# Optimization experiments

Hardware: AMD Instinct MI355X
Metric: run time of the kernel (lower is better)

## Reference

```python
import jax, jax.numpy as jnp
import numpy as np

B = 65536
F = 300                      # length of each frequency response function
SIGMA = 2.0                  # gaussian blur stdev (init arg)
SCALE = 1.0                  # scale_factor
ALPHA = 1.0                  # softlocalmax sharpness (default)
I0, I1 = 100.0, 200.0        # interval passed to __init__
PMAX = F // 2 + 1            # max possible number of strict local maxima (incl. boundary peaks)


def _gauss_kernel(sigma):
    l = int(np.round(3.0 * sigma + 1.0))
    x = np.linspace(-(l - 1.0) / 2.0, (l - 1.0) / 2.0, l)
    k = np.exp(-0.5 * np.square(x) / np.square(sigma))
    return jnp.asarray(k / k.sum(), dtype=jnp.float32)


def _freqs_norm():
    # freqs = arange(1,301) normalized by interval to (-1,1)-centered coords
    f = np.arange(1, F + 1, dtype=np.float32)
    f = (f - I0) / (I1 - I0)
    return jnp.asarray(f * 2.0 - 1.0)


def setup_inputs() -> dict:
    key = jax.random.key(0)
    fr_funcs = jax.random.normal(key, (B, F), dtype=jnp.float32)
    return {"fr_funcs": fr_funcs}


def _forward(fr):
    kernel = _gauss_kernel(SIGMA)
    freqs = _freqs_norm()

    # Gaussian1DBlur: conv1d with symmetric kernel, zero 'same' padding
    f = jax.lax.conv_general_dilated(fr[:, None, :], kernel[None, None, :],
                                     (1,), "SAME")[:, 0, :]  # (B,F)

    # --- peak detection, equivalent to scipy.find_peaks on a width-2
    # symmetric-padded signal: strict interior maxima plus boundary peaks ---
    interior = (f[:, 1:-1] > f[:, :-2]) & (f[:, 1:-1] > f[:, 2:])   # (B,F-2)
    is_peak = jnp.concatenate([f[:, :1] > f[:, 1:2], interior,
                               f[:, -1:] > f[:, -2:-1]], axis=1)    # (B,F)
    P = is_peak.sum(axis=1)                 # number of peaks per row
    nseg = jnp.maximum(P, 1)                # P=0 still yields one segment [0,F-1)

    idx = jnp.arange(F)
    # sorted peak positions, padded with sentinel F
    pos = jnp.sort(jnp.where(is_peak, idx, F), axis=1)[:, :PMAX]    # (B,PMAX)
    # interval dividers = floor midpoints of consecutive peaks (int(start/end) truncation)
    mids = jnp.where(pos[:, 1:] < F, (pos[:, :-1] + pos[:, 1:]) // 2, F)  # (B,PMAX-1)

    # element i in [0,F-1) belongs to segment = #mids <= i  (last index F-1 excluded,
    # exactly as function[int(start):int(end)] with final divider F-1)
    elem_idx = jnp.arange(F - 1)
    seg_id = jax.vmap(lambda m: jnp.searchsorted(m, elem_idx, side="right"))(mids)  # (B,F-1)

    rows = jnp.arange(B)[:, None] * PMAX
    seg_flat = (seg_id + rows).reshape(-1)
    vals = f[:, : F - 1].reshape(-1)
    frq = jnp.broadcast_to(freqs[: F - 1], (B, F - 1)).reshape(-1)
    NS = B * PMAX

    # per-segment stable softmax-weighted frequency (softargmax)
    segmax = jax.ops.segment_max(vals, seg_flat, num_segments=NS)
    w = jnp.exp((vals - segmax[seg_flat]) * ALPHA)
    den = jax.ops.segment_sum(w, seg_flat, num_segments=NS)
    num = jax.ops.segment_sum(w * frq, seg_flat, num_segments=NS)
    sm = (num / jnp.where(den > 0, den, 1.0)).reshape(B, PMAX)      # (B,PMAX)

    valid = jnp.arange(PMAX)[None, :] < nseg[:, None]
    neg_sq = -(sm * sm)                     # midpoint of normalized interval (-1,1) is 0
    in_int = valid & (sm > -1.0) & (sm < 1.0)

    sum_in = jnp.sum(jnp.where(in_int, neg_sq, 0.0), axis=1)
    # no peak in interval: sum of the two largest -(peak-mid)^2 among valid peaks
    top2 = jax.lax.top_k(jnp.where(valid, neg_sq, -jnp.inf), 2)[0]
    top2sum = jnp.sum(jnp.where(jnp.isfinite(top2), top2, 0.0), axis=1)

    return jnp.where(in_int.any(axis=1), sum_in, top2sum) * SCALE   # (B,)


def reference(fr_funcs):
    return _forward(fr_funcs)
```

## Files before the change

### kernel.cpp

```cpp
#include <hip/hip_runtime.h>
#include <cmath>


constexpr int FLEN = 300;
constexpr int RPB  = 4;
constexpr int SMAX = 152;

__global__ __launch_bounds__(256, 8)
void pil_kernel(const float* __restrict__ in, float* __restrict__ out,
                double bk0, double bk1, double bk2, double bk3)
{
    const int w    = threadIdx.x >> 6;
    const int lane = threadIdx.x & 63;
    const int row  = blockIdx.x * RPB + w;

    __shared__ double2        eg_s[RPB][FLEN];
    __shared__ unsigned short ps_s[RPB][SMAX];

    double2*        eg = eg_s[w];
    unsigned short* ps = ps_s[w];

    const float* rin  = in + (size_t)row * FLEN;
    const int    base = lane * 5;
    const bool   act  = (lane < 60);
    const int    bC   = act ? base : 295;

    float r0 = rin[bC+0], r1 = rin[bC+1], r2 = rin[bC+2], r3 = rin[bC+3], r4 = rin[bC+4];
    float l2 = __shfl_up(r2, 1), l3 = __shfl_up(r3, 1), l4 = __shfl_up(r4, 1);
    float h0 = __shfl_down(r0, 1), h1 = __shfl_down(r1, 1), h2 = __shfl_down(r2, 1);
    if (lane == 0)  { l2 = 0.f; l3 = 0.f; l4 = 0.f; }
    if (lane >= 59) { h0 = 0.f; h1 = 0.f; h2 = 0.f; }

    const double d0=(double)l2, d1=(double)l3, d2=(double)l4, d3=(double)r0,
                 d4=(double)r1, d5=(double)r2, d6=(double)r3, d7=(double)r4,
                 d8=(double)h0, d9=(double)h1, d10=(double)h2;
    float f[5];
    f[0] = (float)fma(bk0, d0+d6,  fma(bk1, d1+d5, fma(bk2, d2+d4, bk3*d3)));
    f[1] = (float)fma(bk0, d1+d7,  fma(bk1, d2+d6, fma(bk2, d3+d5, bk3*d4)));
    f[2] = (float)fma(bk0, d2+d8,  fma(bk1, d3+d7, fma(bk2, d4+d6, bk3*d5)));
    f[3] = (float)fma(bk0, d3+d9,  fma(bk1, d4+d8, fma(bk2, d5+d7, bk3*d6)));
    f[4] = (float)fma(bk0, d4+d10, fma(bk1, d5+d9, fma(bk2, d6+d8, bk3*d7)));

    float fm1 = __shfl_up(f[4], 1);
    float fp1 = __shfl_down(f[0], 1);
    if (lane == 0)  fm1 = -__builtin_inff();
    if (lane >= 59) fp1 = -__builtin_inff();

    bool p[5];
    {
        float lft = fm1;
        #pragma unroll
        for (int j = 0; j < 5; ++j) {
            float rgt = (j < 4) ? f[j+1] : fp1;
            p[j] = act && (f[j] > lft) && (f[j] > rgt);
            lft = f[j];
        }
    }

    unsigned long long b0 = __ballot(p[0]), b1 = __ballot(p[1]), b2 = __ballot(p[2]),
                       b3 = __ballot(p[3]), b4 = __ballot(p[4]);
    const unsigned long long below = (1ull << lane) - 1ull;
    int off = __popcll(b0 & below) + __popcll(b1 & below) + __popcll(b2 & below)
            + __popcll(b3 & below) + __popcll(b4 & below);
    const int P = __popcll(b0) + __popcll(b1) + __popcll(b2) + __popcll(b3) + __popcll(b4);
    #pragma unroll
    for (int j = 0; j < 5; ++j)
        if (p[j]) ps[off++] = (unsigned short)(base + j);

    float e5[5], fr5[5];
    double tE = 0.0, tG = 0.0;
    #pragma unroll
    for (int j = 0; j < 5; ++j) {
        int  i = base + j;
        bool v = act && (i < FLEN - 1);
        e5[j]  = v ? __expf(f[j]) : 0.f;
        fr5[j] = fmaf((float)(i - 99), 0.02f, -1.0f);
        tE += (double)e5[j];
        tG  = fma((double)e5[j], (double)fr5[j], tG);
    }

    double sE = tE, sG = tG;
    #pragma unroll
    for (int d = 1; d < 64; d <<= 1) {
        double a = __shfl_up(sE, d), b = __shfl_up(sG, d);
        if (lane >= d) { sE += a; sG += b; }
    }

    double runE = sE - tE, runG = sG - tG;
    if (lane == 63) eg[0] = make_double2(0.0, 0.0);
    #pragma unroll
    for (int j = 0; j < 5; ++j) {
        int i = base + j;
        runE += (double)e5[j];
        runG  = fma((double)e5[j], (double)fr5[j], runG);
        if (act && i <= FLEN - 2)
            eg[i + 1] = make_double2(runE, runG);
    }
    __syncthreads();

    const int nseg = (P > 0) ? P : 1;
    float sum_in = 0.f; int any_in = 0;
    float nsq_l[3]; int nsq_n = 0;
    for (int s = lane; s < nseg; s += 64) {
        int im = (s > 0) ? s - 1 : 0;
        int ip = (s < P - 1) ? s + 1 : im;
        int pm = ps[im], pc = ps[(P > 0) ? s : 0], pn = ps[ip];
        int lo = (s == 0)        ? 0        : ((pm + pc) >> 1);
        int hi = (s == nseg - 1) ? FLEN - 1 : ((pc + pn) >> 1);
        double2 a = eg[lo], b = eg[hi];
        float den = (float)(b.x - a.x);
        float num = (float)(b.y - a.y);
        float sm  = num / den;
        float nsq = -(sm * sm);
        bool  ii  = (sm > -1.0f) && (sm < 1.0f);
        if (ii) { sum_in += nsq; any_in = 1; }
        if (nsq_n < 3) nsq_l[nsq_n] = nsq;
        nsq_n += 1;
    }

    if (__ballot(any_in) != 0ull) {
        #pragma unroll
        for (int d = 32; d >= 1; d >>= 1) sum_in += __shfl_xor(sum_in, d);
        if (lane == 0) out[row] = sum_in;
    } else {
        float m1 = -__builtin_inff(), m2 = -__builtin_inff();
        for (int q = 0; q < nsq_n; ++q) {
            float nsq = nsq_l[q];
            if (nsq > m1) { m2 = m1; m1 = nsq; } else { m2 = fmaxf(m2, nsq); }
        }
        #pragma unroll
        for (int d = 32; d >= 1; d >>= 1) {
            float o1 = __shfl_xor(m1, d);
            float o2 = __shfl_xor(m2, d);
            float n1 = fmaxf(m1, o1);
            float n2 = fmaxf(fminf(m1, o1), fmaxf(m2, o2));
            m1 = n1; m2 = n2;
        }
        if (lane == 0) {
            float t2 = m1 + ((m2 > -__builtin_inff()) ? m2 : 0.0f);
            out[row] = t2;
        }
    }
}

extern "C" void kernel_launch(void* const* d_in, const int* in_sizes, int n_in,
                              void* d_out, int out_size, void* d_ws, size_t ws_size,
                              hipStream_t stream) {
    const float* in  = (const float*)d_in[0];
    float*       out = (float*)d_out;
    const int B = in_sizes[0] / FLEN;

    double k[7], s = 0.0;
    for (int t = 0; t < 7; ++t) {
        double x = -3.0 + (double)t;
        k[t] = exp(-0.5 * x * x / 4.0);
        s += k[t];
    }
    double bk0 = (double)(float)(k[0] / s);
    double bk1 = (double)(float)(k[1] / s);
    double bk2 = (double)(float)(k[2] / s);
    double bk3 = (double)(float)(k[3] / s);

    pil_kernel<<<B / RPB, 256, 0, stream>>>(in, out, bk0, bk1, bk2, bk3);
}
```

Baseline: 126.8 us.

## Replace block barrier with wave-level sync, shrink blocks, use mbcnt offsets

```diff
diff --git a/kernel.cpp b/kernel.cpp
--- a/kernel.cpp
+++ b/kernel.cpp
@@ -3,10 +3,10 @@
 
 
 constexpr int FLEN = 300;
-constexpr int RPB  = 4;
+constexpr int RPB  = 2;
 constexpr int SMAX = 152;
 
-__global__ __launch_bounds__(256, 8)
+__global__ __launch_bounds__(128, 8)
 void pil_kernel(const float* __restrict__ in, float* __restrict__ out,
                 double bk0, double bk1, double bk2, double bk3)
 {
@@ -59,24 +59,34 @@
 
     unsigned long long b0 = __ballot(p[0]), b1 = __ballot(p[1]), b2 = __ballot(p[2]),
                        b3 = __ballot(p[3]), b4 = __ballot(p[4]);
-    const unsigned long long below = (1ull << lane) - 1ull;
-    int off = __popcll(b0 & below) + __popcll(b1 & below) + __popcll(b2 & below)
-            + __popcll(b3 & below) + __popcll(b4 & below);
+    int off = 0;
+    off = __builtin_amdgcn_mbcnt_lo((unsigned)b0, off);
+    off = __builtin_amdgcn_mbcnt_hi((unsigned)(b0 >> 32), off);
+    off = __builtin_amdgcn_mbcnt_lo((unsigned)b1, off);
+    off = __builtin_amdgcn_mbcnt_hi((unsigned)(b1 >> 32), off);
+    off = __builtin_amdgcn_mbcnt_lo((unsigned)b2, off);
+    off = __builtin_amdgcn_mbcnt_hi((unsigned)(b2 >> 32), off);
+    off = __builtin_amdgcn_mbcnt_lo((unsigned)b3, off);
+    off = __builtin_amdgcn_mbcnt_hi((unsigned)(b3 >> 32), off);
+    off = __builtin_amdgcn_mbcnt_lo((unsigned)b4, off);
+    off = __builtin_amdgcn_mbcnt_hi((unsigned)(b4 >> 32), off);
     const int P = __popcll(b0) + __popcll(b1) + __popcll(b2) + __popcll(b3) + __popcll(b4);
     #pragma unroll
     for (int j = 0; j < 5; ++j)
         if (p[j]) ps[off++] = (unsigned short)(base + j);
 
-    float e5[5], fr5[5];
+    double cE[5], cG[5];
     double tE = 0.0, tG = 0.0;
     #pragma unroll
     for (int j = 0; j < 5; ++j) {
         int  i = base + j;
         bool v = act && (i < FLEN - 1);
-        e5[j]  = v ? __expf(f[j]) : 0.f;
-        fr5[j] = fmaf((float)(i - 99), 0.02f, -1.0f);
-        tE += (double)e5[j];
-        tG  = fma((double)e5[j], (double)fr5[j], tG);
+        float e  = v ? __expf(f[j]) : 0.f;
+        float fr = fmaf((float)(i - 99), 0.02f, -1.0f);
+        double de = (double)e;
+        tE += de;
+        tG  = fma(de, (double)fr, tG);
+        cE[j] = tE; cG[j] = tG;
     }
 
     double sE = tE, sG = tG;
@@ -85,18 +95,19 @@
         double a = __shfl_up(sE, d), b = __shfl_up(sG, d);
         if (lane >= d) { sE += a; sG += b; }
     }
+    const double xE = sE - tE, xG = sG - tG;
 
-    double runE = sE - tE, runG = sG - tG;
     if (lane == 63) eg[0] = make_double2(0.0, 0.0);
     #pragma unroll
     for (int j = 0; j < 5; ++j) {
         int i = base + j;
-        runE += (double)e5[j];
-        runG  = fma((double)e5[j], (double)fr5[j], runG);
         if (act && i <= FLEN - 2)
-            eg[i + 1] = make_double2(runE, runG);
+            eg[i + 1] = make_double2(xE + cE[j], xG + cG[j]);
     }
-    __syncthreads();
+
+    __builtin_amdgcn_wave_barrier();
+    __asm__ volatile("s_waitcnt lgkmcnt(0)" ::: "memory");
+    __builtin_amdgcn_wave_barrier();
 
     const int nseg = (P > 0) ? P : 1;
     float sum_in = 0.f; int any_in = 0;
@@ -161,5 +172,5 @@
     double bk2 = (double)(float)(k[2] / s);
     double bk3 = (double)(float)(k[3] / s);
 
-    pil_kernel<<<B / RPB, 256, 0, stream>>>(in, out, bk0, bk1, bk2, bk3);
+    pil_kernel<<<B / RPB, 128, 0, stream>>>(in, out, bk0, bk1, bk2, bk3);
 }
```

New measurement: 126.2 us. About the same (-0.4%).
